# Optimization experiments

Measured on AMD Instinct MI355X. Metric: run time of the kernel, lower is better.

Reference implementation:

```python
import jax, jax.numpy as jnp
import numpy as np

B, S, D, H = 4, 2048, 1024, 16
DH = D // H          # per-head attention size (attention_size // n_heads)
F = 4 * D            # FFN hidden
EPS = 1e-5


def _layer_norm(x, g, b):
    m = jnp.mean(x, axis=-1, keepdims=True)
    v = jnp.mean(jnp.square(x - m), axis=-1, keepdims=True)
    return (x - m) * jax.lax.rsqrt(v + EPS) * g + b


def setup_inputs() -> dict:
    key = jax.random.key(0)
    ks = jax.random.split(key, 12)
    s = 0.02
    x = jax.random.normal(ks[0], (B, S, D), dtype=jnp.float32)
    # causal mask: True = masked (strict upper triangle)
    mask = jnp.broadcast_to(jnp.triu(jnp.ones((S, S), dtype=bool), k=1), (B, S, S))
    wq = jax.random.normal(ks[1], (H, D, DH), dtype=jnp.float32) * s
    wk = jax.random.normal(ks[2], (H, D, DH), dtype=jnp.float32) * s
    wv = jax.random.normal(ks[3], (H, D, DH), dtype=jnp.float32) * s
    wo = jax.random.normal(ks[4], (D, D), dtype=jnp.float32) * s   # attention_size -> embedding_dim
    w1 = jax.random.normal(ks[5], (D, F), dtype=jnp.float32) * s
    b1 = jax.random.normal(ks[6], (F,), dtype=jnp.float32) * s
    w2 = jax.random.normal(ks[7], (F, D), dtype=jnp.float32) * s
    b2 = jax.random.normal(ks[8], (D,), dtype=jnp.float32) * s
    ln1_g = jnp.ones((D,), jnp.float32) + jax.random.normal(ks[9], (D,), jnp.float32) * s
    ln1_b = jax.random.normal(ks[10], (D,), jnp.float32) * s
    ln2_g = jnp.ones((D,), jnp.float32) + jax.random.normal(ks[11], (D,), jnp.float32) * s
    ln2_b = jnp.zeros((D,), jnp.float32)
    return {"x": x, "mask": mask, "wq": wq, "wk": wk, "wv": wv, "wo": wo,
            "w1": w1, "b1": b1, "w2": w2, "b2": b2,
            "ln1_g": ln1_g, "ln1_b": ln1_b, "ln2_g": ln2_g, "ln2_b": ln2_b}


def reference(x, mask, wq, wk, wv, wo, w1, b1, w2, b2, ln1_g, ln1_b, ln2_g, ln2_b):
    # --- self-attention block (pre-norm, residual) ---
    h = _layer_norm(x, ln1_g, ln1_b)                       # [B,S,D]
    q = jnp.einsum('bsd,hde->bhse', h, wq)                 # [B,H,S,DH]
    k = jnp.einsum('bsd,hde->bhse', h, wk)
    v = jnp.einsum('bsd,hde->bhse', h, wv)
    scores = jnp.einsum('bhse,bhte->bhst', q, k)           # [B,H,S,S]
    # faithful to source: mask-fill with -inf, THEN divide by sqrt(head_dim)
    scores = jnp.where(mask[:, None, :, :], -jnp.inf, scores) / jnp.sqrt(jnp.float32(DH))
    p = jax.nn.softmax(scores, axis=-1)
    attn = jnp.einsum('bhst,bhte->bhse', p, v)             # [B,H,S,DH]
    concat = attn.transpose(0, 2, 1, 3).reshape(B, S, D)   # heads concatenated on feature dim
    x = x + concat @ wo
    # --- feed-forward block ---
    h2 = _layer_norm(x, ln2_g, ln2_b)
    ff = jax.nn.gelu(h2 @ w1 + b1, approximate=False) @ w2 + b2
    return x + ff
```

## Files before the change

kernel.cpp:

```cpp
#include <hip/hip_runtime.h>
#include <hip/hip_bf16.h>
#include <math.h>


#define Bz 4
#define Sz 2048
#define Dz 1024
#define Hz 16
#define DHz 64
#define Fz 4096
#define Mz 8192

typedef float f32x4 __attribute__((ext_vector_type(4)));
typedef __bf16 bf16x8 __attribute__((ext_vector_type(8)));
typedef __bf16 bf16x4 __attribute__((ext_vector_type(4)));
typedef short s16x4 __attribute__((ext_vector_type(4)));

#define GLOAD_LDS16(g, l)                                                                   \
  __builtin_amdgcn_global_load_lds((const __attribute__((address_space(1))) unsigned int*)(g), \
                                   (__attribute__((address_space(3))) unsigned int*)(l), 16, 0, 0)

static __device__ __forceinline__ unsigned short f2bu(float f) {
  unsigned int u = __float_as_uint(f);
  u += 0x7fffu + ((u >> 16) & 1u);
  return (unsigned short)(u >> 16);
}

static __device__ __forceinline__ f32x4 mfma32(bf16x8 a, bf16x8 b, f32x4 c) {
  return __builtin_amdgcn_mfma_f32_16x16x32_bf16(a, b, c, 0, 0, 0);
}
static __device__ __forceinline__ f32x4 mfma16(s16x4 a, s16x4 b, f32x4 c) {
#if __has_builtin(__builtin_amdgcn_mfma_f32_16x16x16bf16_1k)
  return __builtin_amdgcn_mfma_f32_16x16x16bf16_1k(a, b, c, 0, 0, 0);
#else
  asm("v_mfma_f32_16x16x16_bf16 %0, %1, %2, %0" : "+v"(c) : "v"(a), "v"(b));
  return c;
#endif
}

template <int OFF>
static __device__ __forceinline__ s16x4 tr16(unsigned addr) {
  s16x4 r;
  asm volatile("ds_read_b64_tr_b16 %0, %1 offset:%2" : "=v"(r) : "v"(addr), "i"(OFF));
  return r;
}


__global__ __launch_bounds__(256) void pack_qkv(
    const float* __restrict__ wq, const float* __restrict__ wk, const float* __restrict__ wv,
    unsigned short* __restrict__ outW)
{
  __shared__ float tile[64][65];
  const int blk = blockIdx.x;
  const int dc = blk & 15;
  const int h  = (blk >> 4) & 15;
  const int p  = blk >> 8;
  const float* w = p == 0 ? wq : (p == 1 ? wk : wv);
  const int tid = threadIdx.x;
#pragma unroll
  for (int i = 0; i < 4; ++i) {
    int idx = i * 256 + tid;
    int dl = idx >> 4;
    int e0 = (idx & 15) * 4;
    const float4 v = *(const float4*)&w[(size_t)(h * 1024 + dc * 64 + dl) * 64 + e0];
    tile[dl][e0 + 0] = v.x; tile[dl][e0 + 1] = v.y;
    tile[dl][e0 + 2] = v.z; tile[dl][e0 + 3] = v.w;
  }
  __syncthreads();
#pragma unroll
  for (int i = 0; i < 4; ++i) {
    int idx = i * 256 + tid;
    int e = idx >> 4;
    int d0 = (idx & 15) * 4;
    ushort4 o;
    o.x = f2bu(tile[d0 + 0][e]); o.y = f2bu(tile[d0 + 1][e]);
    o.z = f2bu(tile[d0 + 2][e]); o.w = f2bu(tile[d0 + 3][e]);
    *(ushort4*)&outW[(size_t)(p * 1024 + h * 64 + e) * 1024 + dc * 64 + d0] = o;
  }
}

__global__ __launch_bounds__(256) void transpose_f32_to_bf16(
    const float* __restrict__ in, unsigned short* __restrict__ out, int R, int C)
{
  __shared__ float tile[32][33];
  int c0 = blockIdx.x * 32, r0 = blockIdx.y * 32;
  int x = threadIdx.x, y = threadIdx.y;
#pragma unroll
  for (int i = 0; i < 32; i += 8)
    tile[y + i][x] = in[(size_t)(r0 + y + i) * C + c0 + x];
  __syncthreads();
#pragma unroll
  for (int i = 0; i < 32; i += 8)
    out[(size_t)(c0 + y + i) * R + r0 + x] = f2bu(tile[x][y + i]);
}


__global__ __launch_bounds__(256) void ln_kernel(
    const float* __restrict__ x, const float* __restrict__ gamma, const float* __restrict__ beta,
    unsigned short* __restrict__ outH)
{
  const int row = blockIdx.x;
  const int tid = threadIdx.x;
  const float4 v = ((const float4*)(x + (size_t)row * Dz))[tid];
  float s = v.x + v.y + v.z + v.w;
  float s2 = v.x * v.x + v.y * v.y + v.z * v.z + v.w * v.w;
#pragma unroll
  for (int o = 32; o > 0; o >>= 1) {
    s += __shfl_xor(s, o);
    s2 += __shfl_xor(s2, o);
  }
  __shared__ float ss[4], ss2[4];
  if ((tid & 63) == 0) { ss[tid >> 6] = s; ss2[tid >> 6] = s2; }
  __syncthreads();
  s = ss[0] + ss[1] + ss[2] + ss[3];
  s2 = ss2[0] + ss2[1] + ss2[2] + ss2[3];
  const float mean = s * (1.0f / Dz);
  const float rstd = rsqrtf(s2 * (1.0f / Dz) - mean * mean + 1e-5f);
  const float4 g4 = ((const float4*)gamma)[tid];
  const float4 b4 = ((const float4*)beta)[tid];
  ushort4 o;
  o.x = f2bu((v.x - mean) * rstd * g4.x + b4.x);
  o.y = f2bu((v.y - mean) * rstd * g4.y + b4.y);
  o.z = f2bu((v.z - mean) * rstd * g4.z + b4.z);
  o.w = f2bu((v.w - mean) * rstd * g4.w + b4.w);
  ((ushort4*)(outH + (size_t)row * Dz))[tid] = o;
}


enum { EPI_BF16 = 0, EPI_GELU_BF16 = 1, EPI_RES_F32 = 2, EPI_BIAS_RES_F32 = 3 };

template <int BN, int EPI>
__global__ __launch_bounds__(512, 2) void gemm256(
    const unsigned short* __restrict__ A,
    const unsigned short* __restrict__ BT,
    int M, int N, int K,
    const float* bias, const float* resid,
    unsigned short* outb, float* outf)
{
  constexpr int BM = 256, BK = 64;
  constexpr int ACH = (BM * BK * 2) / (512 * 16);
  constexpr int BCH = (BN * BK * 2) / (512 * 16);
  constexpr int NCH = ACH + BCH;
  constexpr int NREP = BN / 64;
  __shared__ unsigned short As[2][BM * BK];
  __shared__ unsigned short Bs[2][BN * BK];

  const int tid = threadIdx.x;
  const int lane = tid & 63;
  const int wid = tid >> 6;
  const int wr = wid >> 2;
  const int wc = wid & 3;
  const int rsel = lane & 15;
  const int kgrp = lane >> 4;

  const int nwg = gridDim.x;
  const int bid = blockIdx.x;
  const int id2 = (bid & 7) * (nwg >> 3) + (bid >> 3);
  const int nbx = N / BN;
  const int n0 = (id2 % nbx) * BN;
  const int m0 = (id2 / nbx) * BM;

  f32x4 acc[8][NREP] = {};

  auto issue = [&](int kt, int b) {
    const int kOff = kt * BK;
#pragma unroll
    for (int r = 0; r < ACH; ++r) {
      int gc = r * 512 + tid;
      int row = gc >> 3;
      int kcs = (gc & 7) ^ (row & 7);
      GLOAD_LDS16(A + (size_t)(m0 + row) * K + kOff + kcs * 8, &As[b][gc * 8]);
    }
#pragma unroll
    for (int r = 0; r < BCH; ++r) {
      int gc = r * 512 + tid;
      int row = gc >> 3;
      int kcs = (gc & 7) ^ (row & 7);
      GLOAD_LDS16(BT + (size_t)(n0 + row) * K + kOff + kcs * 8, &Bs[b][gc * 8]);
    }
  };

  auto compute = [&](int b) {
    const unsigned short* Ab = As[b];
    const unsigned short* Bb = Bs[b];
#pragma unroll
    for (int kk = 0; kk < 2; ++kk) {
      bf16x8 af[8], bfr[NREP];
#pragma unroll
      for (int mf = 0; mf < 8; ++mf) {
        int ar = wr * 128 + mf * 16 + rsel;
        af[mf] = *(const bf16x8*)&Ab[ar * 64 + (((kk * 4 + kgrp) ^ (ar & 7)) * 8)];
      }
#pragma unroll
      for (int nf = 0; nf < NREP; ++nf) {
        int br = wc * (BN / 4) + nf * 16 + rsel;
        bfr[nf] = *(const bf16x8*)&Bb[br * 64 + (((kk * 4 + kgrp) ^ (br & 7)) * 8)];
      }
#pragma unroll
      for (int mf = 0; mf < 8; ++mf)
#pragma unroll
        for (int nf = 0; nf < NREP; ++nf)
          acc[mf][nf] = mfma32(af[mf], bfr[nf], acc[mf][nf]);
    }
  };

  const int T = K >> 6;
  issue(0, 0);
  for (int t = 0; t < T; ++t) {
    if (t + 1 < T) {
      issue(t + 1, (t + 1) & 1);
      if constexpr (NCH == 8) asm volatile("s_waitcnt vmcnt(8)" ::: "memory");
      else                    asm volatile("s_waitcnt vmcnt(6)" ::: "memory");
    } else {
      asm volatile("s_waitcnt vmcnt(0)" ::: "memory");
    }
    __builtin_amdgcn_sched_barrier(0);
    __builtin_amdgcn_s_barrier();
    __builtin_amdgcn_sched_barrier(0);
    compute(t & 1);
    __builtin_amdgcn_sched_barrier(0);
    __builtin_amdgcn_s_barrier();
  }

#pragma unroll
  for (int mf = 0; mf < 8; ++mf) {
#pragma unroll
    for (int nf = 0; nf < NREP; ++nf) {
      const int n = n0 + wc * (BN / 4) + nf * 16 + rsel;
#pragma unroll
      for (int j = 0; j < 4; ++j) {
        const int m = m0 + wr * 128 + mf * 16 + kgrp * 4 + j;
        const size_t idx = (size_t)m * N + n;
        float v = acc[mf][nf][j];
        if constexpr (EPI == EPI_BF16) {
          outb[idx] = f2bu(v);
        } else if constexpr (EPI == EPI_GELU_BF16) {
          v += bias[n];
          v = 0.5f * v * (1.0f + erff(v * 0.70710678118654752f));
          outb[idx] = f2bu(v);
        } else if constexpr (EPI == EPI_RES_F32) {
          outf[idx] = v + resid[idx];
        } else {
          outf[idx] = v + bias[n] + resid[idx];
        }
      }
    }
  }
}


__global__ __launch_bounds__(256, 4) void attn_kernel(
    const unsigned short* __restrict__ QKV,
    unsigned short* __restrict__ outA)
{
  __shared__ unsigned short Kt[64 * 64];
  __shared__ unsigned short Vs[64 * 64];
  const int pi = blockIdx.x;
  const int hh = blockIdx.y;
  const int bb = blockIdx.z;
  const int tid = threadIdx.x;
  const int lane = tid & 63;
  const int w = tid >> 6;
  const int rsel = lane & 15;
  const int kgrp = lane >> 4;
  const int qtA = pi, qtB = 31 - pi;
  const int qgA = qtA * 64 + w * 16 + rsel;
  const int qgB = qtB * 64 + w * 16 + rsel;
  const size_t rowQA = (size_t)(bb * Sz + qgA) * 3072 + hh * 64;
  const size_t rowQB = (size_t)(bb * Sz + qgB) * 3072 + hh * 64;

  const bf16x8 qfA0 = *(const bf16x8*)&QKV[rowQA + kgrp * 8];
  const bf16x8 qfA1 = *(const bf16x8*)&QKV[rowQA + 32 + kgrp * 8];
  const bf16x8 qfB0 = *(const bf16x8*)&QKV[rowQB + kgrp * 8];
  const bf16x8 qfB1 = *(const bf16x8*)&QKV[rowQB + 32 + kgrp * 8];

  f32x4 accA[4] = {}, accB[4] = {};
  float mA = -INFINITY, lA = 0.0f, mB = -INFINITY, lB = 0.0f;

  auto vs3 = (__attribute__((address_space(3))) unsigned short*)Vs;
  const unsigned vbase = (unsigned)(uintptr_t)vs3 + (unsigned)lane * 8u;
  constexpr float SCL = 0.18033688011112042f;

  auto proc = [&](const bf16x8& qf0, const bf16x8& qf1, float& mrun, float& lrun,
                  f32x4* accO, s16x4* pb, bool edge, int qg, int kb) {
    f32x4 sc[4];
    __builtin_amdgcn_s_setprio(1);
#pragma unroll
    for (int kf = 0; kf < 4; ++kf) {
      int key = kf * 16 + rsel;
      bf16x8 k0 = *(const bf16x8*)&Kt[key * 64 + ((kgrp ^ (key & 7)) * 8)];
      bf16x8 k1 = *(const bf16x8*)&Kt[key * 64 + (((4 + kgrp) ^ (key & 7)) * 8)];
      f32x4 s = {};
      s = mfma32(k0, qf0, s);
      s = mfma32(k1, qf1, s);
      sc[kf] = s;
    }
    __builtin_amdgcn_s_setprio(0);
    float tmax = -INFINITY;
#pragma unroll
    for (int kf = 0; kf < 4; ++kf)
#pragma unroll
      for (int j = 0; j < 4; ++j) {
        float v = sc[kf][j] * SCL;
        if (edge) {
          int keyg = kb + kf * 16 + kgrp * 4 + j;
          if (keyg > qg) v = -INFINITY;
        }
        sc[kf][j] = v;
        tmax = fmaxf(tmax, v);
      }
    tmax = fmaxf(tmax, __shfl_xor(tmax, 16));
    tmax = fmaxf(tmax, __shfl_xor(tmax, 32));
    if (!__all(tmax <= mrun + 8.0f)) {
      const float mnew = fmaxf(mrun, tmax);
      const float corr = exp2f(mrun - mnew);
      lrun *= corr;
#pragma unroll
      for (int df = 0; df < 4; ++df) accO[df] *= corr;
      mrun = mnew;
    }
    float psum = 0.0f;
#pragma unroll
    for (int kf = 0; kf < 4; ++kf) {
      bf16x4 pv;
#pragma unroll
      for (int j = 0; j < 4; ++j) {
        float e = exp2f(sc[kf][j] - mrun);
        psum += e;
        pv[j] = (__bf16)e;
      }
      pb[kf] = __builtin_bit_cast(s16x4, pv);
    }
    psum += __shfl_xor(psum, 16);
    psum += __shfl_xor(psum, 32);
    lrun += psum;
  };

  for (int kt = 0; kt <= qtB; ++kt) {
    const int kb = kt * 64;
    const bool doA = (kt <= qtA);
    if (kt) __syncthreads();
#pragma unroll
    for (int r = 0; r < 2; ++r) {
      int c = r * 256 + tid;
      int key = c >> 3;
      int dcs = (c & 7) ^ (key & 7);
      GLOAD_LDS16(QKV + (size_t)(bb * Sz + kb + key) * 3072 + 1024 + hh * 64 + dcs * 8,
                  &Kt[c * 8]);
    }
#pragma unroll
    for (int r = 0; r < 2; ++r) {
      int c = r * 256 + tid;
      int key = ((c >> 3) & 15) * 4 + ((c >> 1) & 3);
      int d = (c >> 7) * 16 + (c & 1) * 8;
      GLOAD_LDS16(QKV + (size_t)(bb * Sz + kb + key) * 3072 + 2048 + hh * 64 + d,
                  &Vs[c * 8]);
    }
    __syncthreads();

    s16x4 pbA[4], pbB[4];
    if (doA) proc(qfA0, qfA1, mA, lA, accA, pbA, kt == qtA, qgA, kb);
    proc(qfB0, qfB1, mB, lB, accB, pbB, kt == qtB, qgB, kb);

#pragma unroll
    for (int df = 0; df < 4; ++df) {
      unsigned a = vbase + df * 2048;
      s16x4 vf0 = tr16<0>(a);
      s16x4 vf1 = tr16<512>(a);
      s16x4 vf2 = tr16<1024>(a);
      s16x4 vf3 = tr16<1536>(a);
      asm volatile("s_waitcnt lgkmcnt(0)" ::: "memory");
      __builtin_amdgcn_sched_barrier(0);
      __builtin_amdgcn_s_setprio(1);
      if (doA) {
        accA[df] = mfma16(vf0, pbA[0], accA[df]);
        accA[df] = mfma16(vf1, pbA[1], accA[df]);
        accA[df] = mfma16(vf2, pbA[2], accA[df]);
        accA[df] = mfma16(vf3, pbA[3], accA[df]);
      }
      accB[df] = mfma16(vf0, pbB[0], accB[df]);
      accB[df] = mfma16(vf1, pbB[1], accB[df]);
      accB[df] = mfma16(vf2, pbB[2], accB[df]);
      accB[df] = mfma16(vf3, pbB[3], accB[df]);
      __builtin_amdgcn_s_setprio(0);
    }
  }

  auto epi = [&](const f32x4* accO, float lrun, int qg) {
    const float rl = 1.0f / lrun;
    const size_t orow = (size_t)(bb * Sz + qg) * Dz + hh * 64;
#pragma unroll
    for (int df = 0; df < 4; ++df) {
      s16x4 o;
#pragma unroll
      for (int j = 0; j < 4; ++j) o[j] = (short)f2bu(accO[df][j] * rl);
      *(s16x4*)&outA[orow + df * 16 + kgrp * 4] = o;
    }
  };
  epi(accA, lA, qgA);
  epi(accB, lB, qgB);
}


extern "C" void kernel_launch(void* const* d_in, const int* in_sizes, int n_in,
                              void* d_out, int out_size, void* d_ws, size_t ws_size,
                              hipStream_t stream) {
  const float* x   = (const float*)d_in[0];
  const float* wq  = (const float*)d_in[2];
  const float* wk  = (const float*)d_in[3];
  const float* wv  = (const float*)d_in[4];
  const float* wo  = (const float*)d_in[5];
  const float* w1  = (const float*)d_in[6];
  const float* b1  = (const float*)d_in[7];
  const float* w2  = (const float*)d_in[8];
  const float* b2  = (const float*)d_in[9];
  const float* g1  = (const float*)d_in[10];
  const float* be1 = (const float*)d_in[11];
  const float* g2  = (const float*)d_in[12];
  const float* be2 = (const float*)d_in[13];
  float* out = (float*)d_out;

  char* ws = (char*)d_ws;
  unsigned short* WqkvT = (unsigned short*)(ws);
  unsigned short* WoT   = (unsigned short*)(ws + 6291456);
  unsigned short* W1T   = (unsigned short*)(ws + 8388608);
  unsigned short* W2T   = (unsigned short*)(ws + 16777216);
  unsigned short* hbuf  = (unsigned short*)(ws + 25165824);
  unsigned short* big   = (unsigned short*)(ws + 41943040);

  dim3 tb(32, 8);
  pack_qkv<<<768, 256, 0, stream>>>(wq, wk, wv, WqkvT);
  transpose_f32_to_bf16<<<dim3(32, 32), tb, 0, stream>>>(wo, WoT, 1024, 1024);
  transpose_f32_to_bf16<<<dim3(128, 32), tb, 0, stream>>>(w1, W1T, 1024, 4096);
  transpose_f32_to_bf16<<<dim3(32, 128), tb, 0, stream>>>(w2, W2T, 4096, 1024);

  ln_kernel<<<Mz, 256, 0, stream>>>(x, g1, be1, hbuf);
  gemm256<256, EPI_BF16><<<384, 512, 0, stream>>>(
      hbuf, WqkvT, Mz, 3072, 1024, nullptr, nullptr, big, nullptr);
  attn_kernel<<<dim3(16, 16, 4), 256, 0, stream>>>(big, hbuf);
  gemm256<128, EPI_RES_F32><<<256, 512, 0, stream>>>(
      hbuf, WoT, Mz, 1024, 1024, nullptr, x, nullptr, out);
  ln_kernel<<<Mz, 256, 0, stream>>>(out, g2, be2, hbuf);
  gemm256<256, EPI_GELU_BF16><<<512, 512, 0, stream>>>(
      hbuf, W1T, Mz, Fz, 1024, b1, nullptr, big, nullptr);
  gemm256<128, EPI_BIAS_RES_F32><<<256, 512, 0, stream>>>(
      big, W2T, Mz, 1024, Fz, b2, out, nullptr, out);
}
```

Baseline: 499.8 us.

## Interleave GEMM loads with MFMA phases and process four query tiles per attention block

```diff
diff --git a/kernel.cpp b/kernel.cpp
--- a/kernel.cpp
+++ b/kernel.cpp
@@ -138,9 +138,7 @@
     unsigned short* outb, float* outf)
 {
   constexpr int BM = 256, BK = 64;
-  constexpr int ACH = (BM * BK * 2) / (512 * 16);
   constexpr int BCH = (BN * BK * 2) / (512 * 16);
-  constexpr int NCH = ACH + BCH;
   constexpr int NREP = BN / 64;
   __shared__ unsigned short As[2][BM * BK];
   __shared__ unsigned short Bs[2][BN * BK];
@@ -162,64 +160,79 @@
 
   f32x4 acc[8][NREP] = {};
 
-  auto issue = [&](int kt, int b) {
-    const int kOff = kt * BK;
-#pragma unroll
-    for (int r = 0; r < ACH; ++r) {
-      int gc = r * 512 + tid;
-      int row = gc >> 3;
-      int kcs = (gc & 7) ^ (row & 7);
-      GLOAD_LDS16(A + (size_t)(m0 + row) * K + kOff + kcs * 8, &As[b][gc * 8]);
-    }
-#pragma unroll
-    for (int r = 0; r < BCH; ++r) {
-      int gc = r * 512 + tid;
-      int row = gc >> 3;
-      int kcs = (gc & 7) ^ (row & 7);
-      GLOAD_LDS16(BT + (size_t)(n0 + row) * K + kOff + kcs * 8, &Bs[b][gc * 8]);
-    }
+  auto stA = [&](int kt, int b, int r) {
+    int gc = r * 512 + tid;
+    int row = gc >> 3;
+    int kcs = (gc & 7) ^ (row & 7);
+    GLOAD_LDS16(A + (size_t)(m0 + row) * K + kt * BK + kcs * 8, &As[b][gc * 8]);
   };
-
-  auto compute = [&](int b) {
+  auto stB = [&](int kt, int b, int r) {
+    int gc = r * 512 + tid;
+    int row = gc >> 3;
+    int kcs = (gc & 7) ^ (row & 7);
+    GLOAD_LDS16(BT + (size_t)(n0 + row) * K + kt * BK + kcs * 8, &Bs[b][gc * 8]);
+  };
+
+#pragma unroll
+  for (int r = 0; r < BCH; ++r) stB(0, 0, r);
+  stA(0, 0, 0); stA(0, 0, 2); stA(0, 0, 1); stA(0, 0, 3);
+  asm volatile("s_waitcnt vmcnt(2)" ::: "memory");
+  __builtin_amdgcn_sched_barrier(0);
+  __builtin_amdgcn_s_barrier();
+
+  const int T = K >> 6;
+  for (int t = 0; t < T; ++t) {
+    const int b = t & 1;
+    const bool more = (t + 1 < T);
     const unsigned short* Ab = As[b];
     const unsigned short* Bb = Bs[b];
-#pragma unroll
-    for (int kk = 0; kk < 2; ++kk) {
-      bf16x8 af[8], bfr[NREP];
-#pragma unroll
-      for (int mf = 0; mf < 8; ++mf) {
-        int ar = wr * 128 + mf * 16 + rsel;
-        af[mf] = *(const bf16x8*)&Ab[ar * 64 + (((kk * 4 + kgrp) ^ (ar & 7)) * 8)];
-      }
-#pragma unroll
-      for (int nf = 0; nf < NREP; ++nf) {
-        int br = wc * (BN / 4) + nf * 16 + rsel;
-        bfr[nf] = *(const bf16x8*)&Bb[br * 64 + (((kk * 4 + kgrp) ^ (br & 7)) * 8)];
-      }
-#pragma unroll
-      for (int mf = 0; mf < 8; ++mf)
+    bf16x8 bfr[NREP];
+#pragma unroll
+    for (int p = 0; p < 4; ++p) {
+      const int kk = p >> 1, mh = p & 1;
+      if (mh == 0) {
+#pragma unroll
+        for (int nf = 0; nf < NREP; ++nf) {
+          int br = wc * (BN / 4) + nf * 16 + rsel;
+          bfr[nf] = *(const bf16x8*)&Bb[br * BK + (((kk * 4 + kgrp) ^ (br & 7)) * 8)];
+        }
+      }
+      bf16x8 af[4];
+#pragma unroll
+      for (int q = 0; q < 4; ++q) {
+        int ar = wr * 128 + (mh * 4 + q) * 16 + rsel;
+        af[q] = *(const bf16x8*)&Ab[ar * BK + (((kk * 4 + kgrp) ^ (ar & 7)) * 8)];
+      }
+      if (more) {
+        if constexpr (BN == 256) {
+          if (p == 0)      { stB(t + 1, b ^ 1, 0); stB(t + 1, b ^ 1, 1); }
+          else if (p == 1) { stB(t + 1, b ^ 1, 2); stB(t + 1, b ^ 1, 3); }
+          else if (p == 2) { stA(t + 1, b ^ 1, 0); stA(t + 1, b ^ 1, 2); }
+          else             { stA(t + 1, b ^ 1, 1); stA(t + 1, b ^ 1, 3); }
+        } else {
+          if (p == 0)      { stB(t + 1, b ^ 1, 0); stB(t + 1, b ^ 1, 1); }
+          else if (p == 1) { stA(t + 1, b ^ 1, 0); stA(t + 1, b ^ 1, 2); }
+          else if (p == 2) { stA(t + 1, b ^ 1, 1); stA(t + 1, b ^ 1, 3); }
+        }
+      }
+      if (p == 0 || p == 3) {
+        if (more) asm volatile("s_waitcnt vmcnt(2)" ::: "memory");
+        else      asm volatile("s_waitcnt vmcnt(0)" ::: "memory");
+      }
+      __builtin_amdgcn_sched_barrier(0);
+      __builtin_amdgcn_s_barrier();
+      asm volatile("s_waitcnt lgkmcnt(0)" ::: "memory");
+      __builtin_amdgcn_sched_barrier(0);
+      __builtin_amdgcn_s_setprio(1);
+#pragma unroll
+      for (int q = 0; q < 4; ++q)
 #pragma unroll
         for (int nf = 0; nf < NREP; ++nf)
-          acc[mf][nf] = mfma32(af[mf], bfr[nf], acc[mf][nf]);
-    }
-  };
-
-  const int T = K >> 6;
-  issue(0, 0);
-  for (int t = 0; t < T; ++t) {
-    if (t + 1 < T) {
-      issue(t + 1, (t + 1) & 1);
-      if constexpr (NCH == 8) asm volatile("s_waitcnt vmcnt(8)" ::: "memory");
-      else                    asm volatile("s_waitcnt vmcnt(6)" ::: "memory");
-    } else {
-      asm volatile("s_waitcnt vmcnt(0)" ::: "memory");
-    }
-    __builtin_amdgcn_sched_barrier(0);
-    __builtin_amdgcn_s_barrier();
-    __builtin_amdgcn_sched_barrier(0);
-    compute(t & 1);
-    __builtin_amdgcn_sched_barrier(0);
-    __builtin_amdgcn_s_barrier();
+          acc[mh * 4 + q][nf] = mfma32(af[q], bfr[nf], acc[mh * 4 + q][nf]);
+      __builtin_amdgcn_s_setprio(0);
+      __builtin_amdgcn_sched_barrier(0);
+      __builtin_amdgcn_s_barrier();
+    }
   }
 
 #pragma unroll
@@ -249,13 +262,13 @@
 }
 
 
-__global__ __launch_bounds__(256, 4) void attn_kernel(
+__global__ __launch_bounds__(256, 2) void attn_kernel(
     const unsigned short* __restrict__ QKV,
     unsigned short* __restrict__ outA)
 {
   __shared__ unsigned short Kt[64 * 64];
   __shared__ unsigned short Vs[64 * 64];
-  const int pi = blockIdx.x;
+  const int ii = blockIdx.x;
   const int hh = blockIdx.y;
   const int bb = blockIdx.z;
   const int tid = threadIdx.x;
@@ -263,26 +276,28 @@
   const int w = tid >> 6;
   const int rsel = lane & 15;
   const int kgrp = lane >> 4;
-  const int qtA = pi, qtB = 31 - pi;
-  const int qgA = qtA * 64 + w * 16 + rsel;
-  const int qgB = qtB * 64 + w * 16 + rsel;
-  const size_t rowQA = (size_t)(bb * Sz + qgA) * 3072 + hh * 64;
-  const size_t rowQB = (size_t)(bb * Sz + qgB) * 3072 + hh * 64;
-
-  const bf16x8 qfA0 = *(const bf16x8*)&QKV[rowQA + kgrp * 8];
-  const bf16x8 qfA1 = *(const bf16x8*)&QKV[rowQA + 32 + kgrp * 8];
-  const bf16x8 qfB0 = *(const bf16x8*)&QKV[rowQB + kgrp * 8];
-  const bf16x8 qfB1 = *(const bf16x8*)&QKV[rowQB + 32 + kgrp * 8];
-
-  f32x4 accA[4] = {}, accB[4] = {};
-  float mA = -INFINITY, lA = 0.0f, mB = -INFINITY, lB = 0.0f;
+  const int qt[4] = {ii, 15 - ii, 16 + ii, 31 - ii};
+
+  bf16x8 qf0[4], qf1[4];
+  int qg[4];
+#pragma unroll
+  for (int s = 0; s < 4; ++s) {
+    qg[s] = qt[s] * 64 + w * 16 + rsel;
+    const size_t rowQ = (size_t)(bb * Sz + qg[s]) * 3072 + hh * 64;
+    qf0[s] = *(const bf16x8*)&QKV[rowQ + kgrp * 8];
+    qf1[s] = *(const bf16x8*)&QKV[rowQ + 32 + kgrp * 8];
+  }
+
+  f32x4 accO[4][4] = {};
+  float mr[4] = {-INFINITY, -INFINITY, -INFINITY, -INFINITY};
+  float lr[4] = {0.0f, 0.0f, 0.0f, 0.0f};
 
   auto vs3 = (__attribute__((address_space(3))) unsigned short*)Vs;
   const unsigned vbase = (unsigned)(uintptr_t)vs3 + (unsigned)lane * 8u;
   constexpr float SCL = 0.18033688011112042f;
 
-  auto proc = [&](const bf16x8& qf0, const bf16x8& qf1, float& mrun, float& lrun,
-                  f32x4* accO, s16x4* pb, bool edge, int qg, int kb) {
+  auto proc = [&](const bf16x8& q0, const bf16x8& q1, float& mrun, float& lrun,
+                  f32x4* accS, s16x4* pb, bool edge, int qgs, int kb) {
     f32x4 sc[4];
     __builtin_amdgcn_s_setprio(1);
 #pragma unroll
@@ -291,8 +306,8 @@
       bf16x8 k0 = *(const bf16x8*)&Kt[key * 64 + ((kgrp ^ (key & 7)) * 8)];
       bf16x8 k1 = *(const bf16x8*)&Kt[key * 64 + (((4 + kgrp) ^ (key & 7)) * 8)];
       f32x4 s = {};
-      s = mfma32(k0, qf0, s);
-      s = mfma32(k1, qf1, s);
+      s = mfma32(k0, q0, s);
+      s = mfma32(k1, q1, s);
       sc[kf] = s;
     }
     __builtin_amdgcn_s_setprio(0);
@@ -304,7 +319,7 @@
         float v = sc[kf][j] * SCL;
         if (edge) {
           int keyg = kb + kf * 16 + kgrp * 4 + j;
-          if (keyg > qg) v = -INFINITY;
+          if (keyg > qgs) v = -INFINITY;
         }
         sc[kf][j] = v;
         tmax = fmaxf(tmax, v);
@@ -316,7 +331,7 @@
       const float corr = exp2f(mrun - mnew);
       lrun *= corr;
 #pragma unroll
-      for (int df = 0; df < 4; ++df) accO[df] *= corr;
+      for (int df = 0; df < 4; ++df) accS[df] *= corr;
       mrun = mnew;
     }
     float psum = 0.0f;
@@ -336,9 +351,8 @@
     lrun += psum;
   };
 
-  for (int kt = 0; kt <= qtB; ++kt) {
+  for (int kt = 0; kt <= qt[3]; ++kt) {
     const int kb = kt * 64;
-    const bool doA = (kt <= qtA);
     if (kt) __syncthreads();
 #pragma unroll
     for (int r = 0; r < 2; ++r) {
@@ -358,9 +372,11 @@
     }
     __syncthreads();
 
-    s16x4 pbA[4], pbB[4];
-    if (doA) proc(qfA0, qfA1, mA, lA, accA, pbA, kt == qtA, qgA, kb);
-    proc(qfB0, qfB1, mB, lB, accB, pbB, kt == qtB, qgB, kb);
+    s16x4 pb[4][4];
+#pragma unroll
+    for (int s = 0; s < 4; ++s)
+      if (kt <= qt[s])
+        proc(qf0[s], qf1[s], mr[s], lr[s], accO[s], pb[s], kt == qt[s], qg[s], kb);
 
 #pragma unroll
     for (int df = 0; df < 4; ++df) {
@@ -372,33 +388,31 @@
       asm volatile("s_waitcnt lgkmcnt(0)" ::: "memory");
       __builtin_amdgcn_sched_barrier(0);
       __builtin_amdgcn_s_setprio(1);
-      if (doA) {
-        accA[df] = mfma16(vf0, pbA[0], accA[df]);
-        accA[df] = mfma16(vf1, pbA[1], accA[df]);
-        accA[df] = mfma16(vf2, pbA[2], accA[df]);
-        accA[df] = mfma16(vf3, pbA[3], accA[df]);
-      }
-      accB[df] = mfma16(vf0, pbB[0], accB[df]);
-      accB[df] = mfma16(vf1, pbB[1], accB[df]);
-      accB[df] = mfma16(vf2, pbB[2], accB[df]);
-      accB[df] = mfma16(vf3, pbB[3], accB[df]);
+#pragma unroll
+      for (int s = 0; s < 4; ++s) {
+        if (kt <= qt[s]) {
+          accO[s][df] = mfma16(vf0, pb[s][0], accO[s][df]);
+          accO[s][df] = mfma16(vf1, pb[s][1], accO[s][df]);
+          accO[s][df] = mfma16(vf2, pb[s][2], accO[s][df]);
+          accO[s][df] = mfma16(vf3, pb[s][3], accO[s][df]);
+        }
+      }
       __builtin_amdgcn_s_setprio(0);
     }
   }
 
-  auto epi = [&](const f32x4* accO, float lrun, int qg) {
-    const float rl = 1.0f / lrun;
-    const size_t orow = (size_t)(bb * Sz + qg) * Dz + hh * 64;
+#pragma unroll
+  for (int s = 0; s < 4; ++s) {
+    const float rl = 1.0f / lr[s];
+    const size_t orow = (size_t)(bb * Sz + qg[s]) * Dz + hh * 64;
 #pragma unroll
     for (int df = 0; df < 4; ++df) {
       s16x4 o;
 #pragma unroll
-      for (int j = 0; j < 4; ++j) o[j] = (short)f2bu(accO[df][j] * rl);
+      for (int j = 0; j < 4; ++j) o[j] = (short)f2bu(accO[s][df][j] * rl);
       *(s16x4*)&outA[orow + df * 16 + kgrp * 4] = o;
     }
-  };
-  epi(accA, lA, qgA);
-  epi(accB, lB, qgB);
+  }
 }
 
 
@@ -435,9 +449,9 @@
   transpose_f32_to_bf16<<<dim3(32, 128), tb, 0, stream>>>(w2, W2T, 4096, 1024);
 
   ln_kernel<<<Mz, 256, 0, stream>>>(x, g1, be1, hbuf);
-  gemm256<256, EPI_BF16><<<384, 512, 0, stream>>>(
+  gemm256<128, EPI_BF16><<<768, 512, 0, stream>>>(
       hbuf, WqkvT, Mz, 3072, 1024, nullptr, nullptr, big, nullptr);
-  attn_kernel<<<dim3(16, 16, 4), 256, 0, stream>>>(big, hbuf);
+  attn_kernel<<<dim3(8, 16, 4), 256, 0, stream>>>(big, hbuf);
   gemm256<128, EPI_RES_F32><<<256, 512, 0, stream>>>(
       hbuf, WoT, Mz, 1024, 1024, nullptr, x, nullptr, out);
   ln_kernel<<<Mz, 256, 0, stream>>>(out, g2, be2, hbuf);
```

New measurement: 459.9 us. -8.0%, faster.
